# Kernel optimization log

Measured on AMD Instinct MI355X. Metric: run time of the kernel, lower is better.

Reference implementation:

```python
import jax, jax.numpy as jnp
import numpy as np

H_DIM = 128      # hidden_size == mid_channels == in/out channels
COND = 128       # cond_dim
N_LAYERS = 2     # attention layers
N_EXP = 3        # experts
NUM_PARAMS = H_DIM * H_DIM          # 1x1 kernel: out_c*in_c*1*1
HYPER_HID = NUM_PARAMS // 2         # 8192


def setup_inputs() -> dict:
    key = jax.random.key(0)
    ks = iter(jax.random.split(key, 32))
    s = 0.02
    d = {}
    d["feature"] = jax.random.normal(next(ks), (8, H_DIM, 48, 48), dtype=jnp.float32)
    d["cond_input"] = jax.random.normal(next(ks), (8, COND), dtype=jnp.float32)
    # self-attention params, stacked over layers; weights stored [in,out]
    for name in ("qw", "kw", "vw"):
        d[name] = jax.random.normal(next(ks), (N_LAYERS, H_DIM, H_DIM), dtype=jnp.float32) * s
    for name in ("qb", "kb", "vb"):
        d[name] = jax.random.normal(next(ks), (N_LAYERS, H_DIM), dtype=jnp.float32) * s
    # MoE experts: Linear->ReLU->Linear per expert, stacked over experts
    d["ew1"] = jax.random.normal(next(ks), (N_EXP, H_DIM, H_DIM), dtype=jnp.float32) * s
    d["eb1"] = jax.random.normal(next(ks), (N_EXP, H_DIM), dtype=jnp.float32) * s
    d["ew2"] = jax.random.normal(next(ks), (N_EXP, H_DIM, H_DIM), dtype=jnp.float32) * s
    d["eb2"] = jax.random.normal(next(ks), (N_EXP, H_DIM), dtype=jnp.float32) * s
    d["gw"] = jax.random.normal(next(ks), (H_DIM, N_EXP), dtype=jnp.float32) * s
    d["gb"] = jax.random.normal(next(ks), (N_EXP,), dtype=jnp.float32) * s
    # hypernetwork generating per-sample 1x1 conv weights
    d["hw1"] = jax.random.normal(next(ks), (COND, HYPER_HID), dtype=jnp.float32) * s
    d["hb1"] = jax.random.normal(next(ks), (HYPER_HID,), dtype=jnp.float32) * s
    d["hw2"] = jax.random.normal(next(ks), (HYPER_HID, NUM_PARAMS), dtype=jnp.float32) * s
    d["hb2"] = jax.random.normal(next(ks), (NUM_PARAMS,), dtype=jnp.float32) * s
    return d


def _forward(feature, cond_input, qw, qb, kw, kb, vw, vb,
             ew1, eb1, ew2, eb2, gw, gb, hw1, hb1, hw2, hb2):
    B, C, H, W = feature.shape
    seq = feature.reshape(B, C, H * W).transpose(0, 2, 1)  # [B, S, C]
    scale = 1.0 / jnp.sqrt(jnp.float32(C))
    for l in range(N_LAYERS):
        q = seq @ qw[l] + qb[l]
        k = seq @ kw[l] + kb[l]
        v = seq @ vw[l] + vb[l]
        scores = jnp.einsum("bsc,btc->bst", q, k) * scale  # [B,S,S]
        probs = jax.nn.softmax(scores, axis=-1)
        seq = seq + jnp.einsum("bst,btc->bsc", probs, v)
    # dense mixture of experts
    gate_w = jax.nn.softmax(seq @ gw + gb, axis=-1)                      # [B,S,E]
    h1 = jax.nn.relu(jnp.einsum("bsc,ecd->bsed", seq, ew1) + eb1)        # [B,S,E,H]
    eo = jnp.einsum("bsed,edf->bsef", h1, ew2) + eb2                     # [B,S,E,H]
    moe = jnp.einsum("bseh,bse->bsh", eo, gate_w)                        # [B,S,H]
    g = jax.nn.sigmoid(moe)
    combined = g * moe + (1.0 - g) * seq
    combined = combined.transpose(0, 2, 1).reshape(B, C, H, W)
    # per-sample 1x1 conditional conv (batched as a single einsum)
    wk = jax.nn.relu(cond_input @ hw1 + hb1) @ hw2 + hb2                 # [B, out*in]
    wk = wk.reshape(B, H_DIM, H_DIM)                                     # [B,out_c,in_c]
    cond_out = jnp.einsum("boi,bihw->bohw", wk, combined)
    return combined + cond_out


def reference(feature, cond_input, qw, qb, kw, kb, vw, vb,
              ew1, eb1, ew2, eb2, gw, gb, hw1, hb1, hw2, hb2):
    return _forward(feature, cond_input, qw, qb, kw, kb, vw, vb,
                    ew1, eb1, ew2, eb2, gw, gb, hw1, hb1, hw2, hb2)
```

## Files before the change

### kernel.cpp

```cpp
#include <hip/hip_runtime.h>
#include <cstdint>
#include <cstddef>

#define BATCH 8
#define CDIM 128
#define SEQ 2304
#define NEXP 3
#define HHID 8192
#define NPAR 16384

typedef unsigned short u16;
typedef __attribute__((ext_vector_type(8))) __bf16 bf16x8;
typedef __attribute__((ext_vector_type(4))) float f32x4;

__device__ __forceinline__ unsigned short f2b(float f) {
    union { float f; unsigned int i; } v; v.f = f;
    unsigned int x = v.i;
    unsigned int r = (x + 0x7fffu + ((x >> 16) & 1u)) >> 16;
    return (unsigned short)r;
}
__device__ __forceinline__ float b2f(unsigned short u) {
    union { unsigned int i; float f; } v; v.i = ((unsigned int)u) << 16; return v.f;
}
__device__ __forceinline__ void ld4bf(const u16* p, float* w) {
    uint2 u = *(const uint2*)p;
    w[0] = b2f((unsigned short)(u.x & 0xffffu));
    w[1] = b2f((unsigned short)(u.x >> 16));
    w[2] = b2f((unsigned short)(u.y & 0xffffu));
    w[3] = b2f((unsigned short)(u.y >> 16));
}

__global__ __launch_bounds__(256) void k_transpose(const float* __restrict__ feat,
                                                   float* __restrict__ seq) {
    __shared__ float lt[128][69];
    int b = blockIdx.x, s0 = blockIdx.y * 64, t = threadIdx.x;
    for (int p = 0; p < 8; ++p) {
        int idx = p * 256 + t;
        int c = idx >> 4, k4 = (idx & 15) * 4;
        float4 u = *(const float4*)(feat + (size_t)b * CDIM * SEQ + (size_t)c * SEQ + s0 + k4);
        lt[c][k4 + 0] = u.x; lt[c][k4 + 1] = u.y;
        lt[c][k4 + 2] = u.z; lt[c][k4 + 3] = u.w;
    }
    __syncthreads();
    for (int p = 0; p < 8; ++p) {
        int w = p * 256 + t;
        int s = w >> 5, c4 = (w & 31) * 4;
        float4 o;
        o.x = lt[c4 + 0][s]; o.y = lt[c4 + 1][s];
        o.z = lt[c4 + 2][s]; o.w = lt[c4 + 3][s];
        *(float4*)(seq + ((size_t)b * SEQ + s0 + s) * CDIM + c4) = o;
    }
}

__global__ __launch_bounds__(256) void k_qkv(const float* __restrict__ seq,
        const float* __restrict__ qw, const float* __restrict__ kw, const float* __restrict__ vw,
        const float* __restrict__ qb, const float* __restrict__ kb, const float* __restrict__ vb,
        u16* __restrict__ qB, u16* __restrict__ kB, u16* __restrict__ vT) {
    __shared__ float lseq[32][132];
    __shared__ u16 lwT[128][140];
    int b = blockIdx.x, s0 = blockIdx.y * 32, t = threadIdx.x;
    for (int p = 0; p < 4; ++p) {
        int idx = p * 256 + t;
        int r = idx >> 5, c4 = (idx & 31) * 4;
        *(float4*)(&lseq[r][c4]) = *(const float4*)(seq + ((size_t)b * SEQ + s0 + r) * CDIM + c4);
    }
    for (int mat = 0; mat < 3; ++mat) {
        const float* w = (mat == 0) ? qw : (mat == 1) ? kw : vw;
        __syncthreads();
        for (int p = 0; p < 8; ++p) {
            int idx = p * 256 + t;
            int i = idx >> 4, oc8 = (idx & 15) * 8;
            float4 u0 = *(const float4*)(w + i * CDIM + oc8);
            float4 u1 = *(const float4*)(w + i * CDIM + oc8 + 4);
            lwT[oc8 + 0][i] = f2b(u0.x); lwT[oc8 + 1][i] = f2b(u0.y);
            lwT[oc8 + 2][i] = f2b(u0.z); lwT[oc8 + 3][i] = f2b(u0.w);
            lwT[oc8 + 4][i] = f2b(u1.x); lwT[oc8 + 5][i] = f2b(u1.y);
            lwT[oc8 + 6][i] = f2b(u1.z); lwT[oc8 + 7][i] = f2b(u1.w);
        }
        __syncthreads();
        if (mat < 2) {
            int oc = t & 127, sg = t >> 7;
            const float* bias = (mat == 0) ? qb : kb;
            float acc[16];
            float bv = bias[oc];
            #pragma unroll
            for (int j = 0; j < 16; ++j) acc[j] = bv;
            for (int i = 0; i < CDIM; i += 4) {
                float wf[4]; ld4bf(&lwT[oc][i], wf);
                #pragma unroll
                for (int j = 0; j < 16; ++j) {
                    float4 sv = *(const float4*)(&lseq[sg * 16 + j][i]);
                    acc[j] += sv.x * wf[0] + sv.y * wf[1] + sv.z * wf[2] + sv.w * wf[3];
                }
            }
            u16* outp = (mat == 0) ? qB : kB;
            #pragma unroll
            for (int j = 0; j < 16; ++j)
                outp[((size_t)b * SEQ + s0 + sg * 16 + j) * CDIM + oc] = f2b(acc[j]);
        } else {
            int s = t & 31, og = t >> 5;
            float acc[16];
            #pragma unroll
            for (int j = 0; j < 16; ++j) acc[j] = vb[og * 16 + j];
            for (int i = 0; i < CDIM; i += 4) {
                float4 sv = *(const float4*)(&lseq[s][i]);
                #pragma unroll
                for (int j = 0; j < 16; ++j) {
                    float wf[4]; ld4bf(&lwT[og * 16 + j][i], wf);
                    acc[j] += sv.x * wf[0] + sv.y * wf[1] + sv.z * wf[2] + sv.w * wf[3];
                }
            }
            #pragma unroll
            for (int j = 0; j < 16; ++j) {
                int oc = og * 16 + j;
                vT[(size_t)b * CDIM * SEQ + (size_t)oc * SEQ + s0 + s] = f2b(acc[j]);
            }
        }
    }
}

#define TQ 32
#define TK 64
__global__ __launch_bounds__(128) void k_flash(const u16* __restrict__ qB,
        const u16* __restrict__ kB, const u16* __restrict__ vT,
        float* __restrict__ seq) {
    __shared__ u16 lq[32][136];
    __shared__ u16 lk[64][136];
    __shared__ u16 lvT[128][72];
    __shared__ u16 lsP[32][72];
    int b = blockIdx.x, q0 = blockIdx.y * TQ, t = threadIdx.x;
    int w = t >> 6, lane = t & 63;
    int col = lane & 15, quad = lane >> 4;
    const float scale = 0.08838834764831845f;

    for (int p = 0; p < 4; ++p) {
        int idx = p * 128 + t;
        int r = idx >> 4, c8 = (idx & 15) * 8;
        *(uint4*)(&lq[r][c8]) = *(const uint4*)(qB + ((size_t)b * SEQ + q0 + r) * CDIM + c8);
    }
    f32x4 occ[8];
    f32x4 zero = {0.f, 0.f, 0.f, 0.f};
    #pragma unroll
    for (int ot = 0; ot < 8; ++ot) occ[ot] = zero;
    float rs_r[4] = {0.f, 0.f, 0.f, 0.f};

    for (int kc = 0; kc < SEQ / TK; ++kc) {
        __syncthreads();
        for (int p = 0; p < 8; ++p) {
            int idx = p * 128 + t;
            int r = idx >> 4, c8 = (idx & 15) * 8;
            *(uint4*)(&lk[r][c8]) =
                *(const uint4*)(kB + ((size_t)b * SEQ + kc * TK + r) * CDIM + c8);
        }
        for (int p = 0; p < 8; ++p) {
            int idx = p * 128 + t;
            int cc = idx >> 3, k8 = (idx & 7) * 8;
            *(uint4*)(&lvT[cc][k8]) =
                *(const uint4*)(vT + (size_t)b * CDIM * SEQ + (size_t)cc * SEQ + kc * TK + k8);
        }
        __syncthreads();
        f32x4 sacc[4];
        #pragma unroll
        for (int nt = 0; nt < 4; ++nt) sacc[nt] = zero;
        #pragma unroll
        for (int seg = 0; seg < 4; ++seg) {
            bf16x8 a = *(const bf16x8*)(&lq[w * 16 + col][seg * 32 + quad * 8]);
            #pragma unroll
            for (int nt = 0; nt < 4; ++nt) {
                bf16x8 bb = *(const bf16x8*)(&lk[nt * 16 + col][seg * 32 + quad * 8]);
                sacc[nt] = __builtin_amdgcn_mfma_f32_16x16x32_bf16(a, bb, sacc[nt], 0, 0, 0);
            }
        }
        #pragma unroll
        for (int nt = 0; nt < 4; ++nt) {
            #pragma unroll
            for (int r = 0; r < 4; ++r) {
                float pv = __expf(sacc[nt][r] * scale);
                rs_r[r] += pv;
                lsP[w * 16 + quad * 4 + r][nt * 16 + col] = f2b(pv);
            }
        }
        #pragma unroll
        for (int seg = 0; seg < 2; ++seg) {
            bf16x8 a = *(const bf16x8*)(&lsP[w * 16 + col][seg * 32 + quad * 8]);
            #pragma unroll
            for (int ot = 0; ot < 8; ++ot) {
                bf16x8 bb = *(const bf16x8*)(&lvT[ot * 16 + col][seg * 32 + quad * 8]);
                occ[ot] = __builtin_amdgcn_mfma_f32_16x16x32_bf16(a, bb, occ[ot], 0, 0, 0);
            }
        }
    }
    #pragma unroll
    for (int r = 0; r < 4; ++r) {
        #pragma unroll
        for (int msk = 1; msk < 16; msk <<= 1) rs_r[r] += __shfl_xor(rs_r[r], msk);
    }
    #pragma unroll
    for (int r = 0; r < 4; ++r) {
        float inv = 1.f / rs_r[r];
        int qi = q0 + w * 16 + quad * 4 + r;
        #pragma unroll
        for (int ot = 0; ot < 8; ++ot) {
            int cc = ot * 16 + col;
            size_t adr = ((size_t)b * SEQ + qi) * CDIM + cc;
            seq[adr] += occ[ot][r] * inv;
        }
    }
}

__global__ __launch_bounds__(256) void k_moe(const float* __restrict__ seq,
        const float* __restrict__ ew1, const float* __restrict__ eb1,
        const float* __restrict__ ew2, const float* __restrict__ eb2,
        const float* __restrict__ gw, const float* __restrict__ gb,
        float* __restrict__ comb) {
    __shared__ float lseq[32][132];
    __shared__ float lh1[32][132];
    __shared__ u16 lwT[128][140];
    __shared__ float lgate[32][4];
    int b = blockIdx.x, s0 = blockIdx.y * 32, t = threadIdx.x;
    for (int p = 0; p < 4; ++p) {
        int idx = p * 256 + t;
        int r = idx >> 5, c4 = (idx & 31) * 4;
        *(float4*)(&lseq[r][c4]) = *(const float4*)(seq + ((size_t)b * SEQ + s0 + r) * CDIM + c4);
    }
    __syncthreads();
    if (t < 96) {
        int s = t & 31, e = t / 32;
        float acc = gb[e];
        for (int i = 0; i < CDIM; ++i) acc += lseq[s][i] * gw[i * 3 + e];
        lgate[s][e] = acc;
    }
    __syncthreads();
    if (t < 32) {
        float a0 = lgate[t][0], a1 = lgate[t][1], a2 = lgate[t][2];
        float mx = fmaxf(a0, fmaxf(a1, a2));
        float e0 = __expf(a0 - mx), e1 = __expf(a1 - mx), e2 = __expf(a2 - mx);
        float inv = 1.f / (e0 + e1 + e2);
        lgate[t][0] = e0 * inv; lgate[t][1] = e1 * inv; lgate[t][2] = e2 * inv;
    }
    int oc = t & 127, sg = t >> 7;
    float macc[16];
    #pragma unroll
    for (int j = 0; j < 16; ++j) macc[j] = 0.f;
    for (int e = 0; e < NEXP; ++e) {
        __syncthreads();
        for (int p = 0; p < 8; ++p) {
            int idx = p * 256 + t;
            int i = idx >> 4, oc8 = (idx & 15) * 8;
            const float* wp = ew1 + (size_t)e * CDIM * CDIM + i * CDIM + oc8;
            float4 u0 = *(const float4*)(wp);
            float4 u1 = *(const float4*)(wp + 4);
            lwT[oc8 + 0][i] = f2b(u0.x); lwT[oc8 + 1][i] = f2b(u0.y);
            lwT[oc8 + 2][i] = f2b(u0.z); lwT[oc8 + 3][i] = f2b(u0.w);
            lwT[oc8 + 4][i] = f2b(u1.x); lwT[oc8 + 5][i] = f2b(u1.y);
            lwT[oc8 + 6][i] = f2b(u1.z); lwT[oc8 + 7][i] = f2b(u1.w);
        }
        __syncthreads();
        {
            float acc[16];
            float bv = eb1[e * CDIM + oc];
            #pragma unroll
            for (int j = 0; j < 16; ++j) acc[j] = bv;
            for (int i = 0; i < CDIM; i += 4) {
                float wf[4]; ld4bf(&lwT[oc][i], wf);
                #pragma unroll
                for (int j = 0; j < 16; ++j) {
                    float4 sv = *(const float4*)(&lseq[sg * 16 + j][i]);
                    acc[j] += sv.x * wf[0] + sv.y * wf[1] + sv.z * wf[2] + sv.w * wf[3];
                }
            }
            #pragma unroll
            for (int j = 0; j < 16; ++j) lh1[sg * 16 + j][oc] = fmaxf(acc[j], 0.f);
        }
        __syncthreads();
        for (int p = 0; p < 8; ++p) {
            int idx = p * 256 + t;
            int i = idx >> 4, oc8 = (idx & 15) * 8;
            const float* wp = ew2 + (size_t)e * CDIM * CDIM + i * CDIM + oc8;
            float4 u0 = *(const float4*)(wp);
            float4 u1 = *(const float4*)(wp + 4);
            lwT[oc8 + 0][i] = f2b(u0.x); lwT[oc8 + 1][i] = f2b(u0.y);
            lwT[oc8 + 2][i] = f2b(u0.z); lwT[oc8 + 3][i] = f2b(u0.w);
            lwT[oc8 + 4][i] = f2b(u1.x); lwT[oc8 + 5][i] = f2b(u1.y);
            lwT[oc8 + 6][i] = f2b(u1.z); lwT[oc8 + 7][i] = f2b(u1.w);
        }
        __syncthreads();
        {
            float bv = eb2[e * CDIM + oc];
            float acc[16];
            #pragma unroll
            for (int j = 0; j < 16; ++j) acc[j] = bv;
            for (int i = 0; i < CDIM; i += 4) {
                float wf[4]; ld4bf(&lwT[oc][i], wf);
                #pragma unroll
                for (int j = 0; j < 16; ++j) {
                    float4 hv = *(const float4*)(&lh1[sg * 16 + j][i]);
                    acc[j] += hv.x * wf[0] + hv.y * wf[1] + hv.z * wf[2] + hv.w * wf[3];
                }
            }
            #pragma unroll
            for (int j = 0; j < 16; ++j) macc[j] += lgate[sg * 16 + j][e] * acc[j];
        }
    }
    #pragma unroll
    for (int j = 0; j < 16; ++j) {
        int s = sg * 16 + j;
        float mo = macc[j];
        float g = 1.f / (1.f + __expf(-mo));
        comb[((size_t)b * SEQ + s0 + s) * CDIM + oc] = g * mo + (1.f - g) * lseq[s][oc];
    }
}

__global__ __launch_bounds__(256) void k_h1(const float* __restrict__ cond,
        const float* __restrict__ hw1, const float* __restrict__ hb1,
        float* __restrict__ hh) {
    __shared__ float lcond[8][128];
    int t = threadIdx.x;
    int j = blockIdx.x * 256 + t;
    for (int r = 0; r < 4; ++r) {
        int e = r * 256 + t;
        lcond[e >> 7][e & 127] = cond[e];
    }
    __syncthreads();
    float acc[8];
    float bv = hb1[j];
    #pragma unroll
    for (int bb = 0; bb < 8; ++bb) acc[bb] = bv;
    for (int i = 0; i < CDIM; ++i) {
        float w = hw1[(size_t)i * HHID + j];
        #pragma unroll
        for (int bb = 0; bb < 8; ++bb) acc[bb] += lcond[bb][i] * w;
    }
    #pragma unroll
    for (int bb = 0; bb < 8; ++bb) hh[(size_t)bb * HHID + j] = fmaxf(acc[bb], 0.f);
}

__global__ __launch_bounds__(256) void k_h2init(const float* __restrict__ hb2,
                                                float* __restrict__ wkp) {
    int idx = blockIdx.x * 256 + threadIdx.x;
    wkp[idx] = hb2[idx & (NPAR - 1)];
}

__global__ __launch_bounds__(256) void k_h2(const float* __restrict__ hh,
        const float* __restrict__ hw2, float* __restrict__ wkp) {
    __shared__ float lh[8][256];
    int t = threadIdx.x;
    int n0 = blockIdx.x * 1024 + t * 4;
    int k0 = blockIdx.y * 256;
    for (int p = 0; p < 8; ++p) {
        int idx = p * 256 + t;
        int bb = idx >> 8, k = idx & 255;
        lh[bb][k] = hh[(size_t)bb * HHID + k0 + k];
    }
    __syncthreads();
    f32x4 acc[8];
    f32x4 zero = {0.f, 0.f, 0.f, 0.f};
    #pragma unroll
    for (int bb = 0; bb < 8; ++bb) acc[bb] = zero;
    for (int k = 0; k < 256; ++k) {
        f32x4 w = *(const f32x4*)(hw2 + (size_t)(k0 + k) * NPAR + n0);
        #pragma unroll
        for (int bb = 0; bb < 8; ++bb) acc[bb] += w * lh[bb][k];
    }
    #pragma unroll
    for (int bb = 0; bb < 8; ++bb) {
        #pragma unroll
        for (int j = 0; j < 4; ++j)
            atomicAdd(&wkp[(size_t)bb * NPAR + n0 + j], acc[bb][j]);
    }
}

__global__ __launch_bounds__(256) void k_conv(const float* __restrict__ comb,
        const float* __restrict__ wkp, float* __restrict__ out) {
    __shared__ float lc[32][132];
    int b = blockIdx.x, s0 = blockIdx.y * 32, t = threadIdx.x;
    for (int p = 0; p < 4; ++p) {
        int idx = p * 256 + t;
        int r = idx >> 5, c4 = (idx & 31) * 4;
        *(float4*)(&lc[r][c4]) = *(const float4*)(comb + ((size_t)b * SEQ + s0 + r) * CDIM + c4);
    }
    __syncthreads();
    int s = t & 31, og = t >> 5;
    #pragma unroll
    for (int j = 0; j < 16; ++j) {
        int oc = og * 16 + j;
        const float* wrow = wkp + (size_t)b * NPAR + oc * CDIM;
        float acc = 0.f;
        for (int i = 0; i < CDIM; i += 4) {
            float4 wv = *(const float4*)(wrow + i);
            float4 cv = *(const float4*)(&lc[s][i]);
            acc += wv.x * cv.x + wv.y * cv.y + wv.z * cv.z + wv.w * cv.w;
        }
        out[(size_t)b * CDIM * SEQ + (size_t)oc * SEQ + s0 + s] = lc[s][oc] + acc;
    }
}

extern "C" void kernel_launch(void* const* d_in, const int* in_sizes, int n_in,
                              void* d_out, int out_size, void* d_ws, size_t ws_size,
                              hipStream_t stream) {
    (void)in_sizes; (void)n_in; (void)out_size; (void)ws_size;
    const float* feat = (const float*)d_in[0];
    const float* cond = (const float*)d_in[1];
    const float* qw = (const float*)d_in[2];
    const float* kw = (const float*)d_in[3];
    const float* vw = (const float*)d_in[4];
    const float* qb = (const float*)d_in[5];
    const float* kb = (const float*)d_in[6];
    const float* vb = (const float*)d_in[7];
    const float* ew1 = (const float*)d_in[8];
    const float* eb1 = (const float*)d_in[9];
    const float* ew2 = (const float*)d_in[10];
    const float* eb2 = (const float*)d_in[11];
    const float* gw = (const float*)d_in[12];
    const float* gb = (const float*)d_in[13];
    const float* hw1 = (const float*)d_in[14];
    const float* hb1 = (const float*)d_in[15];
    const float* hw2 = (const float*)d_in[16];
    const float* hb2 = (const float*)d_in[17];
    float* out = (float*)d_out;

    char* ws = (char*)d_ws;
    float* seq  = (float*)(ws);
    float* comb = (float*)(ws + 9437184);
    u16* qBuf   = (u16*)(ws + 18874368);
    u16* kBuf   = (u16*)(ws + 23592960);
    u16* vTbuf  = (u16*)(ws + 28311552);
    float* hh   = (float*)(ws + 33030144);
    float* wkp  = (float*)(ws + 33292288);

    k_transpose<<<dim3(8, 36), 256, 0, stream>>>(feat, seq);
    for (int l = 0; l < 2; ++l) {
        k_qkv<<<dim3(8, 72), 256, 0, stream>>>(seq,
                qw + l * CDIM * CDIM, kw + l * CDIM * CDIM, vw + l * CDIM * CDIM,
                qb + l * CDIM, kb + l * CDIM, vb + l * CDIM,
                qBuf, kBuf, vTbuf);
        k_flash<<<dim3(8, 72), 128, 0, stream>>>(qBuf, kBuf, vTbuf, seq);
    }
    k_moe<<<dim3(8, 72), 256, 0, stream>>>(seq, ew1, eb1, ew2, eb2, gw, gb, comb);
    k_h1<<<dim3(32), 256, 0, stream>>>(cond, hw1, hb1, hh);
    k_h2init<<<dim3(512), 256, 0, stream>>>(hb2, wkp);
    k_h2<<<dim3(16, 32), 256, 0, stream>>>(hh, hw2, wkp);
    k_conv<<<dim3(8, 72), 256, 0, stream>>>(comb, wkp, out);
}
```

Measured before the change: 1.358 ms.

## Use MFMA for QKV and MoE projections, pretranspose weights, prefetch flash tiles

A new prep kernel converts the attention and expert weights to transposed bf16 once per call. The QKV and MoE kernels switch from scalar fp32 FMA loops to bf16 MFMA over 64-row tiles, and register-prefetch the next weight matrix while the current one is used. The flash kernel moves to 64-query blocks with 256 threads and double-buffers K/V tiles in registers. Grids shrink to half the blocks, which lowers occupancy, and the MoE inputs and hidden activations are now rounded to bf16, which may reduce accuracy.

Result: no change. 1.344 ms (-1.0%).

```diff
diff --git a/kernel.cpp b/kernel.cpp
--- a/kernel.cpp
+++ b/kernel.cpp
@@ -8,6 +8,7 @@
 #define NEXP 3
 #define HHID 8192
 #define NPAR 16384
+#define TK 64
 
 typedef unsigned short u16;
 typedef __attribute__((ext_vector_type(8))) __bf16 bf16x8;
@@ -22,12 +23,57 @@
 __device__ __forceinline__ float b2f(unsigned short u) {
     union { unsigned int i; float f; } v; v.i = ((unsigned int)u) << 16; return v.f;
 }
-__device__ __forceinline__ void ld4bf(const u16* p, float* w) {
-    uint2 u = *(const uint2*)p;
-    w[0] = b2f((unsigned short)(u.x & 0xffffu));
-    w[1] = b2f((unsigned short)(u.x >> 16));
-    w[2] = b2f((unsigned short)(u.y & 0xffffu));
-    w[3] = b2f((unsigned short)(u.y >> 16));
+
+__device__ __forceinline__ void loadw(const u16* __restrict__ wsrc, int t, uint4* r) {
+    #pragma unroll
+    for (int j = 0; j < 8; ++j) {
+        int idx = j * 256 + t;
+        int oc = idx >> 4, i8 = (idx & 15) * 8;
+        r[j] = *(const uint4*)(wsrc + oc * CDIM + i8);
+    }
+}
+__device__ __forceinline__ void storew(u16 (*lw)[136], int t, const uint4* r) {
+    #pragma unroll
+    for (int j = 0; j < 8; ++j) {
+        int idx = j * 256 + t;
+        int oc = idx >> 4, i8 = (idx & 15) * 8;
+        *(uint4*)(&lw[oc][i8]) = r[j];
+    }
+}
+
+__global__ __launch_bounds__(256) void k_wprep(const float* __restrict__ qw,
+        const float* __restrict__ kw, const float* __restrict__ vw,
+        const float* __restrict__ ew1, const float* __restrict__ ew2,
+        u16* __restrict__ wTa, u16* __restrict__ wTm) {
+    __shared__ float lt[64][132];
+    int bid = blockIdx.x, t = threadIdx.x;
+    const float* src; u16* dst;
+    if (bid < 6) {
+        int l = bid / 3, m = bid % 3;
+        src = ((m == 0) ? qw : (m == 1) ? kw : vw) + l * CDIM * CDIM;
+        dst = wTa + (size_t)bid * CDIM * CDIM;
+    } else {
+        int q = bid - 6; int e = q >> 1, m = q & 1;
+        src = (m ? ew2 : ew1) + (size_t)e * CDIM * CDIM;
+        dst = wTm + (size_t)q * CDIM * CDIM;
+    }
+    for (int h = 0; h < 2; ++h) {
+        if (h) __syncthreads();
+        for (int p = 0; p < 8; ++p) {
+            int idx = p * 256 + t;
+            int r = idx >> 5, c4 = (idx & 31) * 4;
+            *(float4*)(&lt[r][c4]) = *(const float4*)(src + (h * 64 + r) * CDIM + c4);
+        }
+        __syncthreads();
+        for (int p = 0; p < 8; ++p) {
+            int idx = p * 256 + t;
+            int oc = idx >> 4, i4 = (idx & 15) * 4;
+            uint2 o;
+            o.x = (unsigned int)f2b(lt[i4 + 0][oc]) | ((unsigned int)f2b(lt[i4 + 1][oc]) << 16);
+            o.y = (unsigned int)f2b(lt[i4 + 2][oc]) | ((unsigned int)f2b(lt[i4 + 3][oc]) << 16);
+            *(uint2*)(dst + (size_t)oc * CDIM + h * 64 + i4) = o;
+        }
+    }
 }
 
 __global__ __launch_bounds__(256) void k_transpose(const float* __restrict__ feat,
@@ -53,90 +99,107 @@
 }
 
 __global__ __launch_bounds__(256) void k_qkv(const float* __restrict__ seq,
-        const float* __restrict__ qw, const float* __restrict__ kw, const float* __restrict__ vw,
+        const u16* __restrict__ wT,
         const float* __restrict__ qb, const float* __restrict__ kb, const float* __restrict__ vb,
         u16* __restrict__ qB, u16* __restrict__ kB, u16* __restrict__ vT) {
-    __shared__ float lseq[32][132];
-    __shared__ u16 lwT[128][140];
-    int b = blockIdx.x, s0 = blockIdx.y * 32, t = threadIdx.x;
-    for (int p = 0; p < 4; ++p) {
+    __shared__ __align__(16) u16 lsb[64][136];
+    __shared__ __align__(16) u16 lw[128][136];
+    u16 (*lvs)[80] = (u16 (*)[80])lw;
+    int b = blockIdx.x, s0 = blockIdx.y * 64, t = threadIdx.x;
+    int w = t >> 6, lane = t & 63, col = lane & 15, quad = lane >> 4;
+
+    uint4 wra[8], wrb[8];
+    loadw(wT, t, wra);
+    for (int p = 0; p < 8; ++p) {
         int idx = p * 256 + t;
         int r = idx >> 5, c4 = (idx & 31) * 4;
-        *(float4*)(&lseq[r][c4]) = *(const float4*)(seq + ((size_t)b * SEQ + s0 + r) * CDIM + c4);
-    }
+        float4 u = *(const float4*)(seq + ((size_t)b * SEQ + s0 + r) * CDIM + c4);
+        uint2 o;
+        o.x = (unsigned int)f2b(u.x) | ((unsigned int)f2b(u.y) << 16);
+        o.y = (unsigned int)f2b(u.z) | ((unsigned int)f2b(u.w) << 16);
+        *(uint2*)(&lsb[r][c4]) = o;
+    }
+    __syncthreads();
+    bf16x8 af[4];
+    #pragma unroll
+    for (int seg = 0; seg < 4; ++seg)
+        af[seg] = *(const bf16x8*)(&lsb[w * 16 + col][seg * 32 + quad * 8]);
+
+    #pragma unroll
     for (int mat = 0; mat < 3; ++mat) {
-        const float* w = (mat == 0) ? qw : (mat == 1) ? kw : vw;
+        if (mat > 0) __syncthreads();
+        storew(lw, t, (mat & 1) ? wrb : wra);
+        if (mat == 0) loadw(wT + 16384, t, wrb);
+        if (mat == 1) loadw(wT + 32768, t, wra);
         __syncthreads();
-        for (int p = 0; p < 8; ++p) {
-            int idx = p * 256 + t;
-            int i = idx >> 4, oc8 = (idx & 15) * 8;
-            float4 u0 = *(const float4*)(w + i * CDIM + oc8);
-            float4 u1 = *(const float4*)(w + i * CDIM + oc8 + 4);
-            lwT[oc8 + 0][i] = f2b(u0.x); lwT[oc8 + 1][i] = f2b(u0.y);
-            lwT[oc8 + 2][i] = f2b(u0.z); lwT[oc8 + 3][i] = f2b(u0.w);
-            lwT[oc8 + 4][i] = f2b(u1.x); lwT[oc8 + 5][i] = f2b(u1.y);
-            lwT[oc8 + 6][i] = f2b(u1.z); lwT[oc8 + 7][i] = f2b(u1.w);
-        }
-        __syncthreads();
+        const float* bias = (mat == 0) ? qb : (mat == 1) ? kb : vb;
+        f32x4 acc[8];
+        #pragma unroll
+        for (int nt = 0; nt < 8; ++nt) {
+            float bv = bias[nt * 16 + col];
+            acc[nt] = (f32x4){bv, bv, bv, bv};
+        }
+        #pragma unroll
+        for (int nt = 0; nt < 8; ++nt) {
+            #pragma unroll
+            for (int seg = 0; seg < 4; ++seg) {
+                bf16x8 bf = *(const bf16x8*)(&lw[nt * 16 + col][seg * 32 + quad * 8]);
+                acc[nt] = __builtin_amdgcn_mfma_f32_16x16x32_bf16(af[seg], bf, acc[nt], 0, 0, 0);
+            }
+        }
         if (mat < 2) {
-            int oc = t & 127, sg = t >> 7;
-            const float* bias = (mat == 0) ? qb : kb;
-            float acc[16];
-            float bv = bias[oc];
-            #pragma unroll
-            for (int j = 0; j < 16; ++j) acc[j] = bv;
-            for (int i = 0; i < CDIM; i += 4) {
-                float wf[4]; ld4bf(&lwT[oc][i], wf);
-                #pragma unroll
-                for (int j = 0; j < 16; ++j) {
-                    float4 sv = *(const float4*)(&lseq[sg * 16 + j][i]);
-                    acc[j] += sv.x * wf[0] + sv.y * wf[1] + sv.z * wf[2] + sv.w * wf[3];
-                }
-            }
             u16* outp = (mat == 0) ? qB : kB;
             #pragma unroll
-            for (int j = 0; j < 16; ++j)
-                outp[((size_t)b * SEQ + s0 + sg * 16 + j) * CDIM + oc] = f2b(acc[j]);
+            for (int nt = 0; nt < 8; ++nt)
+                #pragma unroll
+                for (int r = 0; r < 4; ++r)
+                    outp[((size_t)b * SEQ + s0 + w * 16 + quad * 4 + r) * CDIM + nt * 16 + col] =
+                        f2b(acc[nt][r]);
         } else {
-            int s = t & 31, og = t >> 5;
-            float acc[16];
-            #pragma unroll
-            for (int j = 0; j < 16; ++j) acc[j] = vb[og * 16 + j];
-            for (int i = 0; i < CDIM; i += 4) {
-                float4 sv = *(const float4*)(&lseq[s][i]);
-                #pragma unroll
-                for (int j = 0; j < 16; ++j) {
-                    float wf[4]; ld4bf(&lwT[og * 16 + j][i], wf);
-                    acc[j] += sv.x * wf[0] + sv.y * wf[1] + sv.z * wf[2] + sv.w * wf[3];
-                }
-            }
-            #pragma unroll
-            for (int j = 0; j < 16; ++j) {
-                int oc = og * 16 + j;
-                vT[(size_t)b * CDIM * SEQ + (size_t)oc * SEQ + s0 + s] = f2b(acc[j]);
-            }
-        }
-    }
-}
-
-#define TQ 32
-#define TK 64
-__global__ __launch_bounds__(128) void k_flash(const u16* __restrict__ qB,
+            __syncthreads();
+            #pragma unroll
+            for (int nt = 0; nt < 8; ++nt)
+                #pragma unroll
+                for (int r = 0; r < 4; ++r)
+                    lvs[nt * 16 + col][w * 16 + quad * 4 + r] = f2b(acc[nt][r]);
+            __syncthreads();
+            for (int p = 0; p < 4; ++p) {
+                int idx = p * 256 + t;
+                int oc = idx >> 3, s8 = (idx & 7) * 8;
+                uint4 vv = *(const uint4*)(&lvs[oc][s8]);
+                *(uint4*)(vT + ((size_t)b * CDIM + oc) * SEQ + s0 + s8) = vv;
+            }
+        }
+    }
+}
+
+__global__ __launch_bounds__(256) void k_flash(const u16* __restrict__ qB,
         const u16* __restrict__ kB, const u16* __restrict__ vT,
         float* __restrict__ seq) {
-    __shared__ u16 lq[32][136];
-    __shared__ u16 lk[64][136];
-    __shared__ u16 lvT[128][72];
-    __shared__ u16 lsP[32][72];
-    int b = blockIdx.x, q0 = blockIdx.y * TQ, t = threadIdx.x;
-    int w = t >> 6, lane = t & 63;
-    int col = lane & 15, quad = lane >> 4;
+    __shared__ __align__(16) u16 lq[64][136];
+    __shared__ __align__(16) u16 lk[64][136];
+    __shared__ __align__(16) u16 lvT[128][72];
+    __shared__ __align__(16) u16 lsP[64][72];
+    int b = blockIdx.x, q0 = blockIdx.y * 64, t = threadIdx.x;
+    int w = t >> 6, lane = t & 63, col = lane & 15, quad = lane >> 4;
     const float scale = 0.08838834764831845f;
-
-    for (int p = 0; p < 4; ++p) {
-        int idx = p * 128 + t;
+    size_t bS = (size_t)b * SEQ;
+    size_t bCS = (size_t)b * CDIM * SEQ;
+
+    uint4 kr[2][4], vr[2][4];
+    #pragma unroll
+    for (int j = 0; j < 4; ++j) {
+        int idx = j * 256 + t;
         int r = idx >> 4, c8 = (idx & 15) * 8;
-        *(uint4*)(&lq[r][c8]) = *(const uint4*)(qB + ((size_t)b * SEQ + q0 + r) * CDIM + c8);
+        kr[0][j] = *(const uint4*)(kB + (bS + r) * CDIM + c8);
+        int cc = idx >> 3, k8 = (idx & 7) * 8;
+        vr[0][j] = *(const uint4*)(vT + bCS + (size_t)cc * SEQ + k8);
+    }
+    #pragma unroll
+    for (int j = 0; j < 4; ++j) {
+        int idx = j * 256 + t;
+        int r = idx >> 4, c8 = (idx & 15) * 8;
+        *(uint4*)(&lq[r][c8]) = *(const uint4*)(qB + (bS + q0 + r) * CDIM + c8);
     }
     f32x4 occ[8];
     f32x4 zero = {0.f, 0.f, 0.f, 0.f};
@@ -144,49 +207,60 @@
     for (int ot = 0; ot < 8; ++ot) occ[ot] = zero;
     float rs_r[4] = {0.f, 0.f, 0.f, 0.f};
 
-    for (int kc = 0; kc < SEQ / TK; ++kc) {
-        __syncthreads();
-        for (int p = 0; p < 8; ++p) {
-            int idx = p * 128 + t;
-            int r = idx >> 4, c8 = (idx & 15) * 8;
-            *(uint4*)(&lk[r][c8]) =
-                *(const uint4*)(kB + ((size_t)b * SEQ + kc * TK + r) * CDIM + c8);
-        }
-        for (int p = 0; p < 8; ++p) {
-            int idx = p * 128 + t;
-            int cc = idx >> 3, k8 = (idx & 7) * 8;
-            *(uint4*)(&lvT[cc][k8]) =
-                *(const uint4*)(vT + (size_t)b * CDIM * SEQ + (size_t)cc * SEQ + kc * TK + k8);
-        }
-        __syncthreads();
-        f32x4 sacc[4];
-        #pragma unroll
-        for (int nt = 0; nt < 4; ++nt) sacc[nt] = zero;
-        #pragma unroll
-        for (int seg = 0; seg < 4; ++seg) {
-            bf16x8 a = *(const bf16x8*)(&lq[w * 16 + col][seg * 32 + quad * 8]);
+    for (int it = 0; it < SEQ / TK / 2; ++it) {
+        #pragma unroll
+        for (int half = 0; half < 2; ++half) {
+            int kc = it * 2 + half;
+            __syncthreads();
+            #pragma unroll
+            for (int j = 0; j < 4; ++j) {
+                int idx = j * 256 + t;
+                int r = idx >> 4, c8 = (idx & 15) * 8;
+                *(uint4*)(&lk[r][c8]) = kr[half][j];
+                int cc = idx >> 3, k8 = (idx & 7) * 8;
+                *(uint4*)(&lvT[cc][k8]) = vr[half][j];
+            }
+            if (kc + 1 < SEQ / TK) {
+                #pragma unroll
+                for (int j = 0; j < 4; ++j) {
+                    int idx = j * 256 + t;
+                    int r = idx >> 4, c8 = (idx & 15) * 8;
+                    kr[half ^ 1][j] = *(const uint4*)(kB + (bS + (kc + 1) * TK + r) * CDIM + c8);
+                    int cc = idx >> 3, k8 = (idx & 7) * 8;
+                    vr[half ^ 1][j] =
+                        *(const uint4*)(vT + bCS + (size_t)cc * SEQ + (kc + 1) * TK + k8);
+                }
+            }
+            __syncthreads();
+            f32x4 sacc[4];
+            #pragma unroll
+            for (int nt = 0; nt < 4; ++nt) sacc[nt] = zero;
+            #pragma unroll
+            for (int seg = 0; seg < 4; ++seg) {
+                bf16x8 a = *(const bf16x8*)(&lq[w * 16 + col][seg * 32 + quad * 8]);
+                #pragma unroll
+                for (int nt = 0; nt < 4; ++nt) {
+                    bf16x8 bb = *(const bf16x8*)(&lk[nt * 16 + col][seg * 32 + quad * 8]);
+                    sacc[nt] = __builtin_amdgcn_mfma_f32_16x16x32_bf16(a, bb, sacc[nt], 0, 0, 0);
+                }
+            }
             #pragma unroll
             for (int nt = 0; nt < 4; ++nt) {
-                bf16x8 bb = *(const bf16x8*)(&lk[nt * 16 + col][seg * 32 + quad * 8]);
-                sacc[nt] = __builtin_amdgcn_mfma_f32_16x16x32_bf16(a, bb, sacc[nt], 0, 0, 0);
-            }
-        }
-        #pragma unroll
-        for (int nt = 0; nt < 4; ++nt) {
-            #pragma unroll
-            for (int r = 0; r < 4; ++r) {
-                float pv = __expf(sacc[nt][r] * scale);
-                rs_r[r] += pv;
-                lsP[w * 16 + quad * 4 + r][nt * 16 + col] = f2b(pv);
-            }
-        }
-        #pragma unroll
-        for (int seg = 0; seg < 2; ++seg) {
-            bf16x8 a = *(const bf16x8*)(&lsP[w * 16 + col][seg * 32 + quad * 8]);
-            #pragma unroll
-            for (int ot = 0; ot < 8; ++ot) {
-                bf16x8 bb = *(const bf16x8*)(&lvT[ot * 16 + col][seg * 32 + quad * 8]);
-                occ[ot] = __builtin_amdgcn_mfma_f32_16x16x32_bf16(a, bb, occ[ot], 0, 0, 0);
+                #pragma unroll
+                for (int r = 0; r < 4; ++r) {
+                    float pv = __expf(sacc[nt][r] * scale);
+                    rs_r[r] += pv;
+                    lsP[w * 16 + quad * 4 + r][nt * 16 + col] = f2b(pv);
+                }
+            }
+            #pragma unroll
+            for (int seg = 0; seg < 2; ++seg) {
+                bf16x8 a = *(const bf16x8*)(&lsP[w * 16 + col][seg * 32 + quad * 8]);
+                #pragma unroll
+                for (int ot = 0; ot < 8; ++ot) {
+                    bf16x8 bb = *(const bf16x8*)(&lvT[ot * 16 + col][seg * 32 + quad * 8]);
+                    occ[ot] = __builtin_amdgcn_mfma_f32_16x16x32_bf16(a, bb, occ[ot], 0, 0, 0);
+                }
             }
         }
     }
@@ -209,105 +283,120 @@
 }
 
 __global__ __launch_bounds__(256) void k_moe(const float* __restrict__ seq,
-        const float* __restrict__ ew1, const float* __restrict__ eb1,
-        const float* __restrict__ ew2, const float* __restrict__ eb2,
+        const u16* __restrict__ wTm,
+        const float* __restrict__ eb1, const float* __restrict__ eb2,
         const float* __restrict__ gw, const float* __restrict__ gb,
         float* __restrict__ comb) {
-    __shared__ float lseq[32][132];
-    __shared__ float lh1[32][132];
-    __shared__ u16 lwT[128][140];
-    __shared__ float lgate[32][4];
-    int b = blockIdx.x, s0 = blockIdx.y * 32, t = threadIdx.x;
-    for (int p = 0; p < 4; ++p) {
+    __shared__ __align__(16) u16 lsb[64][136];
+    __shared__ __align__(16) u16 lw[128][136];
+    __shared__ float lgate[64][4];
+    int b = blockIdx.x, s0 = blockIdx.y * 64, t = threadIdx.x;
+    int w = t >> 6, lane = t & 63, col = lane & 15, quad = lane >> 4;
+
+    uint4 wra[8], wrb[8];
+    loadw(wTm, t, wra);
+    for (int p = 0; p < 8; ++p) {
         int idx = p * 256 + t;
         int r = idx >> 5, c4 = (idx & 31) * 4;
-        *(float4*)(&lseq[r][c4]) = *(const float4*)(seq + ((size_t)b * SEQ + s0 + r) * CDIM + c4);
-    }
-    __syncthreads();
-    if (t < 96) {
-        int s = t & 31, e = t / 32;
+        float4 u = *(const float4*)(seq + ((size_t)b * SEQ + s0 + r) * CDIM + c4);
+        uint2 o;
+        o.x = (unsigned int)f2b(u.x) | ((unsigned int)f2b(u.y) << 16);
+        o.y = (unsigned int)f2b(u.z) | ((unsigned int)f2b(u.w) << 16);
+        *(uint2*)(&lsb[r][c4]) = o;
+    }
+    __syncthreads();
+    if (t < 192) {
+        int e = t >> 6, s = t & 63;
         float acc = gb[e];
-        for (int i = 0; i < CDIM; ++i) acc += lseq[s][i] * gw[i * 3 + e];
+        for (int i = 0; i < CDIM; ++i) acc += b2f(lsb[s][i]) * gw[i * 3 + e];
         lgate[s][e] = acc;
     }
-    __syncthreads();
-    if (t < 32) {
+    bf16x8 af[4];
+    #pragma unroll
+    for (int seg = 0; seg < 4; ++seg)
+        af[seg] = *(const bf16x8*)(&lsb[w * 16 + col][seg * 32 + quad * 8]);
+    __syncthreads();
+    if (t < 64) {
         float a0 = lgate[t][0], a1 = lgate[t][1], a2 = lgate[t][2];
         float mx = fmaxf(a0, fmaxf(a1, a2));
         float e0 = __expf(a0 - mx), e1 = __expf(a1 - mx), e2 = __expf(a2 - mx);
         float inv = 1.f / (e0 + e1 + e2);
         lgate[t][0] = e0 * inv; lgate[t][1] = e1 * inv; lgate[t][2] = e2 * inv;
     }
-    int oc = t & 127, sg = t >> 7;
-    float macc[16];
-    #pragma unroll
-    for (int j = 0; j < 16; ++j) macc[j] = 0.f;
+    f32x4 macc[8];
+    f32x4 zero = {0.f, 0.f, 0.f, 0.f};
+    #pragma unroll
+    for (int nt = 0; nt < 8; ++nt) macc[nt] = zero;
+
+    #pragma unroll
     for (int e = 0; e < NEXP; ++e) {
         __syncthreads();
-        for (int p = 0; p < 8; ++p) {
-            int idx = p * 256 + t;
-            int i = idx >> 4, oc8 = (idx & 15) * 8;
-            const float* wp = ew1 + (size_t)e * CDIM * CDIM + i * CDIM + oc8;
-            float4 u0 = *(const float4*)(wp);
-            float4 u1 = *(const float4*)(wp + 4);
-            lwT[oc8 + 0][i] = f2b(u0.x); lwT[oc8 + 1][i] = f2b(u0.y);
-            lwT[oc8 + 2][i] = f2b(u0.z); lwT[oc8 + 3][i] = f2b(u0.w);
-            lwT[oc8 + 4][i] = f2b(u1.x); lwT[oc8 + 5][i] = f2b(u1.y);
-            lwT[oc8 + 6][i] = f2b(u1.z); lwT[oc8 + 7][i] = f2b(u1.w);
-        }
+        storew(lw, t, wra);
+        loadw(wTm + (size_t)(2 * e + 1) * 16384, t, wrb);
         __syncthreads();
         {
-            float acc[16];
-            float bv = eb1[e * CDIM + oc];
-            #pragma unroll
-            for (int j = 0; j < 16; ++j) acc[j] = bv;
-            for (int i = 0; i < CDIM; i += 4) {
-                float wf[4]; ld4bf(&lwT[oc][i], wf);
-                #pragma unroll
-                for (int j = 0; j < 16; ++j) {
-                    float4 sv = *(const float4*)(&lseq[sg * 16 + j][i]);
-                    acc[j] += sv.x * wf[0] + sv.y * wf[1] + sv.z * wf[2] + sv.w * wf[3];
+            f32x4 acc[8];
+            #pragma unroll
+            for (int nt = 0; nt < 8; ++nt) {
+                float bv = eb1[e * CDIM + nt * 16 + col];
+                acc[nt] = (f32x4){bv, bv, bv, bv};
+            }
+            #pragma unroll
+            for (int nt = 0; nt < 8; ++nt) {
+                #pragma unroll
+                for (int seg = 0; seg < 4; ++seg) {
+                    bf16x8 bf = *(const bf16x8*)(&lw[nt * 16 + col][seg * 32 + quad * 8]);
+                    acc[nt] = __builtin_amdgcn_mfma_f32_16x16x32_bf16(af[seg], bf, acc[nt], 0, 0, 0);
                 }
             }
             #pragma unroll
-            for (int j = 0; j < 16; ++j) lh1[sg * 16 + j][oc] = fmaxf(acc[j], 0.f);
+            for (int nt = 0; nt < 8; ++nt)
+                #pragma unroll
+                for (int r = 0; r < 4; ++r)
+                    lsb[w * 16 + quad * 4 + r][nt * 16 + col] = f2b(fmaxf(acc[nt][r], 0.f));
         }
         __syncthreads();
-        for (int p = 0; p < 8; ++p) {
-            int idx = p * 256 + t;
-            int i = idx >> 4, oc8 = (idx & 15) * 8;
-            const float* wp = ew2 + (size_t)e * CDIM * CDIM + i * CDIM + oc8;
-            float4 u0 = *(const float4*)(wp);
-            float4 u1 = *(const float4*)(wp + 4);
-            lwT[oc8 + 0][i] = f2b(u0.x); lwT[oc8 + 1][i] = f2b(u0.y);
-            lwT[oc8 + 2][i] = f2b(u0.z); lwT[oc8 + 3][i] = f2b(u0.w);
-            lwT[oc8 + 4][i] = f2b(u1.x); lwT[oc8 + 5][i] = f2b(u1.y);
-            lwT[oc8 + 6][i] = f2b(u1.z); lwT[oc8 + 7][i] = f2b(u1.w);
-        }
+        storew(lw, t, wrb);
+        if (e < 2) loadw(wTm + (size_t)(2 * e + 2) * 16384, t, wra);
         __syncthreads();
         {
-            float bv = eb2[e * CDIM + oc];
-            float acc[16];
-            #pragma unroll
-            for (int j = 0; j < 16; ++j) acc[j] = bv;
-            for (int i = 0; i < CDIM; i += 4) {
-                float wf[4]; ld4bf(&lwT[oc][i], wf);
-                #pragma unroll
-                for (int j = 0; j < 16; ++j) {
-                    float4 hv = *(const float4*)(&lh1[sg * 16 + j][i]);
-                    acc[j] += hv.x * wf[0] + hv.y * wf[1] + hv.z * wf[2] + hv.w * wf[3];
+            bf16x8 a2[4];
+            #pragma unroll
+            for (int seg = 0; seg < 4; ++seg)
+                a2[seg] = *(const bf16x8*)(&lsb[w * 16 + col][seg * 32 + quad * 8]);
+            f32x4 acc2[8];
+            #pragma unroll
+            for (int nt = 0; nt < 8; ++nt) {
+                float bv = eb2[e * CDIM + nt * 16 + col];
+                acc2[nt] = (f32x4){bv, bv, bv, bv};
+            }
+            #pragma unroll
+            for (int nt = 0; nt < 8; ++nt) {
+                #pragma unroll
+                for (int seg = 0; seg < 4; ++seg) {
+                    bf16x8 bf = *(const bf16x8*)(&lw[nt * 16 + col][seg * 32 + quad * 8]);
+                    acc2[nt] = __builtin_amdgcn_mfma_f32_16x16x32_bf16(a2[seg], bf, acc2[nt], 0, 0, 0);
                 }
             }
-            #pragma unroll
-            for (int j = 0; j < 16; ++j) macc[j] += lgate[sg * 16 + j][e] * acc[j];
-        }
-    }
-    #pragma unroll
-    for (int j = 0; j < 16; ++j) {
-        int s = sg * 16 + j;
-        float mo = macc[j];
-        float g = 1.f / (1.f + __expf(-mo));
-        comb[((size_t)b * SEQ + s0 + s) * CDIM + oc] = g * mo + (1.f - g) * lseq[s][oc];
+            float gv[4];
+            #pragma unroll
+            for (int r = 0; r < 4; ++r) gv[r] = lgate[w * 16 + quad * 4 + r][e];
+            #pragma unroll
+            for (int nt = 0; nt < 8; ++nt)
+                #pragma unroll
+                for (int r = 0; r < 4; ++r) macc[nt][r] += gv[r] * acc2[nt][r];
+        }
+    }
+    #pragma unroll
+    for (int nt = 0; nt < 8; ++nt) {
+        #pragma unroll
+        for (int r = 0; r < 4; ++r) {
+            float mo = macc[nt][r];
+            float g = 1.f / (1.f + __expf(-mo));
+            size_t adr = ((size_t)b * SEQ + s0 + w * 16 + quad * 4 + r) * CDIM + nt * 16 + col;
+            float sv = seq[adr];
+            comb[adr] = g * mo + (1.f - g) * sv;
+        }
     }
 }
 
@@ -427,16 +516,17 @@
     u16* vTbuf  = (u16*)(ws + 28311552);
     float* hh   = (float*)(ws + 33030144);
     float* wkp  = (float*)(ws + 33292288);
-
+    u16* wTa    = (u16*)(ws + 33816576);
+    u16* wTm    = (u16*)(ws + 34013184);
+
+    k_wprep<<<dim3(12), 256, 0, stream>>>(qw, kw, vw, ew1, ew2, wTa, wTm);
     k_transpose<<<dim3(8, 36), 256, 0, stream>>>(feat, seq);
     for (int l = 0; l < 2; ++l) {
-        k_qkv<<<dim3(8, 72), 256, 0, stream>>>(seq,
-                qw + l * CDIM * CDIM, kw + l * CDIM * CDIM, vw + l * CDIM * CDIM,
-                qb + l * CDIM, kb + l * CDIM, vb + l * CDIM,
-                qBuf, kBuf, vTbuf);
-        k_flash<<<dim3(8, 72), 128, 0, stream>>>(qBuf, kBuf, vTbuf, seq);
-    }
-    k_moe<<<dim3(8, 72), 256, 0, stream>>>(seq, ew1, eb1, ew2, eb2, gw, gb, comb);
+        k_qkv<<<dim3(8, 36), 256, 0, stream>>>(seq, wTa + (size_t)l * 3 * 16384,
+                qb + l * CDIM, kb + l * CDIM, vb + l * CDIM, qBuf, kBuf, vTbuf);
+        k_flash<<<dim3(8, 36), 256, 0, stream>>>(qBuf, kBuf, vTbuf, seq);
+    }
+    k_moe<<<dim3(8, 36), 256, 0, stream>>>(seq, wTm, eb1, eb2, gw, gb, comb);
     k_h1<<<dim3(32), 256, 0, stream>>>(cond, hw1, hb1, hh);
     k_h2init<<<dim3(512), 256, 0, stream>>>(hb2, wkp);
     k_h2<<<dim3(16, 32), 256, 0, stream>>>(hh, hw2, wkp);
```
